# Performance work log

Hardware: AMD Instinct MI355X
Metric: run time of the kernel (lower is better)

The kernel has to match this reference:

```python
import jax, jax.numpy as jnp
import numpy as np

DIM = 1024
HID = 2048
E = 8
K = 2
INV_SQRT2 = 1.0 / 1.41421356237


def setup_inputs() -> dict:
    key = jax.random.key(0)
    ks = jax.random.split(key, 10)
    s = lambda fan_in: 1.0 / np.sqrt(fan_in)
    return {
        "x": jax.random.normal(ks[0], (4, 2048, DIM), dtype=jnp.float32),
        "gate_w": jax.random.uniform(ks[1], (DIM, E), jnp.float32, -s(DIM), s(DIM)),
        "gate_b": jnp.zeros((E,), jnp.float32),
        "w1": jax.random.uniform(ks[2], (E, DIM, HID), jnp.float32, -s(DIM), s(DIM)),
        "b1": jnp.zeros((E, HID), jnp.float32),
        "w2": jax.random.uniform(ks[3], (E, DIM, HID), jnp.float32, -s(DIM), s(DIM)),
        "b2": jnp.zeros((E, HID), jnp.float32),
        "w3": jax.random.uniform(ks[4], (E, HID, DIM), jnp.float32, -s(HID), s(HID)),
        "b3": jnp.zeros((E, DIM), jnp.float32),
    }


def reference(x, gate_w, gate_b, w1, b1, w2, b2, w3, b3):
    # Gating
    logits = jnp.einsum("bsd,de->bse", x, gate_w) + gate_b          # [b,s,E]
    scores = jax.nn.softmax(logits, axis=-1)
    topk_scores, topk_idx = jax.lax.top_k(scores, K)                  # [b,s,K]

    # Load-balance (entropy) loss over mean expert usage
    usage = scores.mean(axis=(0, 1))                                   # [E]
    lb_loss = -(usage * jnp.log(usage + 1e-9)).sum()

    # Per-token combine weight for each expert: score if expert in top-k else 0
    onehot = jax.nn.one_hot(topk_idx, E, dtype=x.dtype)               # [b,s,K,E]
    comb = (topk_scores[..., None] * onehot).sum(axis=2)              # [b,s,E]

    # SwiGLU experts (batched over E via einsum)
    h = jnp.einsum("bsd,edh->ebsh", x, w1) + b1[:, None, None, :]
    g = jax.nn.silu(jnp.einsum("bsd,edh->ebsh", x, w2) + b2[:, None, None, :])
    eo = jnp.einsum("ebsh,ehd->ebsd", h * g, w3) + b3[:, None, None, :]
    eo = eo * INV_SQRT2

    # Weighted combine (zero weight where expert not selected)
    out = jnp.einsum("ebsd,bse->bsd", eo, comb)
    return out, lb_loss
```

## Files before the change

kernel.cpp:

```cpp
#include <hip/hip_runtime.h>
#include <cstdio>

#define NTOK 8192
#define DIM 1024
#define HID 2048
#define NE 8
#define NPAIR (NTOK * 2)

typedef __attribute__((ext_vector_type(8))) short bf16x8;
typedef __attribute__((ext_vector_type(4))) float f32x4;

typedef const __attribute__((address_space(1))) void* gas_ptr;
typedef __attribute__((address_space(3))) void* las_ptr;

__device__ __forceinline__ void async16(const void* g, void* s) {
  __builtin_amdgcn_global_load_lds((gas_ptr)g, (las_ptr)s, 16, 0, 0);
}

__device__ __forceinline__ unsigned short f2bf(float f) {
  unsigned int u = __float_as_uint(f);
  u = (u + 0x7fff + ((u >> 16) & 1)) >> 16;
  return (unsigned short)u;
}

__device__ __forceinline__ float bf2f(unsigned short u) {
  return __uint_as_float((unsigned int)u << 16);
}


__global__ __launch_bounds__(256) void prep_kernel(
    const float* __restrict__ w1, const float* __restrict__ w2,
    const float* __restrict__ w3, unsigned short* __restrict__ w1bt,
    unsigned short* __restrict__ w2bt, unsigned short* __restrict__ w3bt) {
  const int z = blockIdx.y;
  const int m = z >> 3, e = z & 7;
  int R, C;
  const float* in;
  unsigned short* outp;
  if (m == 0)      { R = DIM; C = HID; in = w1; outp = w1bt; }
  else if (m == 1) { R = DIM; C = HID; in = w2; outp = w2bt; }
  else             { R = HID; C = DIM; in = w3; outp = w3bt; }
  in += (size_t)e * DIM * HID;
  outp += (size_t)e * DIM * HID;

  const int tilesx = C >> 5;
  const int c0 = (blockIdx.x % tilesx) * 32;
  const int r0 = (blockIdx.x / tilesx) * 32;

  __shared__ float tile[32][33];
  const int c = threadIdx.x & 31, rr = threadIdx.x >> 5;
#pragma unroll
  for (int i = 0; i < 4; i++) {
    const int r = rr + i * 8;
    tile[r][c] = in[(size_t)(r0 + r) * C + c0 + c];
  }
  __syncthreads();
#pragma unroll
  for (int i = 0; i < 4; i++) {
    const int cc2 = rr + i * 8;
    outp[(size_t)(c0 + cc2) * R + r0 + c] = f2bf(tile[c][cc2]);
  }
}

__global__ __launch_bounds__(256) void gate_kernel(
    const float* __restrict__ x, const float* __restrict__ gw,
    const float* __restrict__ gb, unsigned short* __restrict__ xb,
    float* __restrict__ scores, int* __restrict__ route_e,
    float* __restrict__ route_w) {
  __shared__ float sgwT[NE][DIM];
  const int tid = threadIdx.x;
#pragma unroll
  for (int i = 0; i < 8; i++) {
    const int j = i * 256 + tid;
    const float4 v = ((const float4*)gw)[j];
    const int d = j >> 1, e0 = (j & 1) * 4;
    sgwT[e0 + 0][d] = v.x; sgwT[e0 + 1][d] = v.y;
    sgwT[e0 + 2][d] = v.z; sgwT[e0 + 3][d] = v.w;
  }
  __syncthreads();

  const int wv = tid >> 6, lane = tid & 63;
  const int t = blockIdx.x * 4 + wv;
  float acc[NE] = {0.f, 0.f, 0.f, 0.f, 0.f, 0.f, 0.f, 0.f};
  const float4* x4 = (const float4*)(x + (size_t)t * DIM);
#pragma unroll
  for (int i = 0; i < 4; i++) {
    const float4 xv = x4[i * 64 + lane];
    const int d4 = i * 64 + lane;
    ushort4 xbv;
    xbv.x = f2bf(xv.x); xbv.y = f2bf(xv.y);
    xbv.z = f2bf(xv.z); xbv.w = f2bf(xv.w);
    *(ushort4*)(xb + (size_t)t * DIM + d4 * 4) = xbv;
#pragma unroll
    for (int e = 0; e < NE; e++) {
      const float4 wv4 = *(const float4*)&sgwT[e][d4 * 4];
      acc[e] += xv.x * wv4.x + xv.y * wv4.y + xv.z * wv4.z + xv.w * wv4.w;
    }
  }
#pragma unroll
  for (int e = 0; e < NE; e++)
#pragma unroll
    for (int s = 32; s; s >>= 1) acc[e] += __shfl_xor(acc[e], s, 64);

  if (lane == 0) {
    float l[NE], m = -1e30f;
#pragma unroll
    for (int e = 0; e < NE; e++) { l[e] = acc[e] + gb[e]; m = fmaxf(m, l[e]); }
    float p[NE], sum = 0.f;
#pragma unroll
    for (int e = 0; e < NE; e++) { p[e] = __expf(l[e] - m); sum += p[e]; }
    const float inv = 1.f / sum;
    float s[NE];
#pragma unroll
    for (int e = 0; e < NE; e++) { s[e] = p[e] * inv; scores[t * NE + e] = s[e]; }
    int i1 = 0;
    for (int e = 1; e < NE; e++) if (s[e] > s[i1]) i1 = e;
    int i2 = -1;
    for (int e = 0; e < NE; e++) {
      if (e == i1) continue;
      if (i2 < 0 || s[e] > s[i2]) i2 = e;
    }
    route_e[t * 2] = i1; route_e[t * 2 + 1] = i2;
    route_w[t * 2] = s[i1]; route_w[t * 2 + 1] = s[i2];
  }
}

__global__ void finalize_kernel(const float* __restrict__ scores,
                                const int* __restrict__ route_e,
                                int* __restrict__ ctrl,
                                float* __restrict__ out_lb) {
  __shared__ float red[1024];
  __shared__ int hist[NE];
  const int tid = threadIdx.x;
  if (tid < NE) hist[tid] = 0;
  const int e = tid & 7, row = tid >> 3;
  float s = 0.f;
  for (int i = 0; i < 64; i++) s += scores[(size_t)(row + i * 128) * NE + e];
  red[tid] = s;
  __syncthreads();
#pragma unroll
  for (int i = 0; i < 16; i++)
    atomicAdd(&hist[route_e[i * 1024 + tid]], 1);
  for (int st = 512; st >= 8; st >>= 1) {
    __syncthreads();
    if (tid < st) red[tid] += red[tid + st];
  }
  __syncthreads();
  if (tid == 0) {
    float lb = 0.f;
    for (int ee = 0; ee < NE; ee++) {
      const float u = red[ee] * (1.f / 8192.f);
      lb -= u * __logf(u + 1e-9f);
    }
    *out_lb = lb;
    int o = 0;
    for (int ee = 0; ee < NE; ee++) {
      ctrl[ee] = hist[ee];
      ctrl[8 + ee] = o;
      ctrl[17 + ee] = o;
      o += hist[ee];
    }
    ctrl[16] = o;
  }
}

__global__ void scatter_kernel(const int* __restrict__ route_e,
                               const float* __restrict__ route_w,
                               int* __restrict__ ctrl,
                               int* __restrict__ tok_list,
                               float* __restrict__ pair_w,
                               int* __restrict__ pair_pos) {
  const int t = blockIdx.x * 256 + threadIdx.x;
  if (t >= NTOK) return;
#pragma unroll
  for (int k = 0; k < 2; k++) {
    const int e = route_e[t * 2 + k];
    const int p = atomicAdd(&ctrl[17 + e], 1);
    tok_list[p] = t;
    pair_w[p] = route_w[t * 2 + k] * 0.70710678118654752f;
    pair_pos[t * 2 + k] = p;
  }
}

__global__ __launch_bounds__(512) void stage1_kernel(
    const unsigned short* __restrict__ xb, const unsigned short* __restrict__ w1bt,
    const unsigned short* __restrict__ w2bt, const float* __restrict__ b1,
    const float* __restrict__ b2, const int* __restrict__ tok_list,
    const int* __restrict__ ctrl, unsigned short* __restrict__ act) {
  const int e = blockIdx.z;
  const int cnt = ctrl[e];
  const int ytile = blockIdx.y;
  if (ytile * 256 >= cnt) return;
  const int off = ctrl[8 + e];
  const int rows = min(256, cnt - ytile * 256);
  const int h0 = blockIdx.x * 128;

  __shared__ unsigned short sX[2][256 * 64];
  __shared__ unsigned short sW1[2][128 * 64];
  __shared__ unsigned short sW2[2][128 * 64];

  const int tid = threadIdx.x;
  const int wv = tid >> 6, lane = tid & 63;
  const int rr = tid >> 3;
  const int c8 = ((tid & 7) ^ (rr & 7)) * 8;

  const unsigned short* w1p = w1bt + (size_t)e * HID * DIM + (size_t)h0 * DIM;
  const unsigned short* w2p = w2bt + (size_t)e * HID * DIM + (size_t)h0 * DIM;
  const unsigned short* gx[4];
  const unsigned short* gw1[2];
  const unsigned short* gw2[2];
#pragma unroll
  for (int r = 0; r < 4; r++)
    gx[r] = xb + (size_t)tok_list[off + ytile * 256 + min(rr + r * 64, rows - 1)] * DIM + c8;
#pragma unroll
  for (int r = 0; r < 2; r++) {
    gw1[r] = w1p + (size_t)(rr + r * 64) * DIM + c8;
    gw2[r] = w2p + (size_t)(rr + r * 64) * DIM + c8;
  }

  f32x4 ah[8][2], ag[8][2];
#pragma unroll
  for (int i = 0; i < 8; i++)
#pragma unroll
    for (int j = 0; j < 2; j++) {
      ah[i][j] = (f32x4){0.f, 0.f, 0.f, 0.f};
      ag[i][j] = (f32x4){0.f, 0.f, 0.f, 0.f};
    }

  const int wr = wv >> 2, wc = wv & 3;
  const int l15 = lane & 15, q = lane >> 4, r7 = lane & 7;

#pragma unroll
  for (int r = 0; r < 4; r++) {
    async16(gx[r], sX[0] + (r * 512 + wv * 64) * 8);
    gx[r] += 64;
  }
#pragma unroll
  for (int r = 0; r < 2; r++) {
    async16(gw1[r], sW1[0] + (r * 512 + wv * 64) * 8);
    async16(gw2[r], sW2[0] + (r * 512 + wv * 64) * 8);
    gw1[r] += 64; gw2[r] += 64;
  }
  __syncthreads();

  const int NT = DIM / 64;
  for (int t = 0; t < NT; t++) {
    const int cur = t & 1;
    if (t + 1 < NT) {
#pragma unroll
      for (int r = 0; r < 4; r++) {
        async16(gx[r], sX[cur ^ 1] + (r * 512 + wv * 64) * 8);
        gx[r] += 64;
      }
#pragma unroll
      for (int r = 0; r < 2; r++) {
        async16(gw1[r], sW1[cur ^ 1] + (r * 512 + wv * 64) * 8);
        async16(gw2[r], sW2[cur ^ 1] + (r * 512 + wv * 64) * 8);
        gw1[r] += 64; gw2[r] += 64;
      }
    }
#pragma unroll
    for (int kk = 0; kk < 2; kk++) {
      const int pch = ((kk * 4 + q) ^ r7) * 8;
      bf16x8 bx[8], a1[2], a2[2];
#pragma unroll
      for (int i = 0; i < 8; i++)
        bx[i] = *(const bf16x8*)(sX[cur] + (wr * 128 + i * 16 + l15) * 64 + pch);
#pragma unroll
      for (int j = 0; j < 2; j++) {
        a1[j] = *(const bf16x8*)(sW1[cur] + (wc * 32 + j * 16 + l15) * 64 + pch);
        a2[j] = *(const bf16x8*)(sW2[cur] + (wc * 32 + j * 16 + l15) * 64 + pch);
      }
#pragma unroll
      for (int i = 0; i < 8; i++)
#pragma unroll
        for (int j = 0; j < 2; j++) {
          ah[i][j] = __builtin_amdgcn_mfma_f32_16x16x32_bf16(a1[j], bx[i], ah[i][j], 0, 0, 0);
          ag[i][j] = __builtin_amdgcn_mfma_f32_16x16x32_bf16(a2[j], bx[i], ag[i][j], 0, 0, 0);
        }
    }
    __syncthreads();
  }

  f32x4 b1v[2], b2v[2];
#pragma unroll
  for (int j = 0; j < 2; j++) {
    const int hc = h0 + wc * 32 + j * 16 + q * 4;
    b1v[j] = *(const f32x4*)(b1 + e * HID + hc);
    b2v[j] = *(const f32x4*)(b2 + e * HID + hc);
  }
#pragma unroll
  for (int i = 0; i < 8; i++) {
    const int trow = wr * 128 + i * 16 + l15;
    if (trow < rows) {
      const size_t gp = (size_t)(off + ytile * 256 + trow) * HID;
#pragma unroll
      for (int j = 0; j < 2; j++) {
        const int hc = h0 + wc * 32 + j * 16 + q * 4;
        ushort4 o;
        {
          const float hh = ah[i][j][0] + b1v[j][0];
          const float gg = ag[i][j][0] + b2v[j][0];
          o.x = f2bf(hh * (gg / (1.f + __expf(-gg))));
        }
        {
          const float hh = ah[i][j][1] + b1v[j][1];
          const float gg = ag[i][j][1] + b2v[j][1];
          o.y = f2bf(hh * (gg / (1.f + __expf(-gg))));
        }
        {
          const float hh = ah[i][j][2] + b1v[j][2];
          const float gg = ag[i][j][2] + b2v[j][2];
          o.z = f2bf(hh * (gg / (1.f + __expf(-gg))));
        }
        {
          const float hh = ah[i][j][3] + b1v[j][3];
          const float gg = ag[i][j][3] + b2v[j][3];
          o.w = f2bf(hh * (gg / (1.f + __expf(-gg))));
        }
        *(ushort4*)(act + gp + hc) = o;
      }
    }
  }
}

__global__ __launch_bounds__(512) void stage2s_kernel(
    const unsigned short* __restrict__ act, const unsigned short* __restrict__ w3bt,
    const float* __restrict__ b3, const float* __restrict__ pair_w,
    const int* __restrict__ ctrl, unsigned short* __restrict__ pair_out) {
  const int e = blockIdx.z;
  const int cnt = ctrl[e];
  const int ytile = blockIdx.y;
  if (ytile * 256 >= cnt) return;
  const int off = ctrl[8 + e];
  const int rows = min(256, cnt - ytile * 256);
  const int d0 = blockIdx.x * 256;
  const int rbase = off + ytile * 256;

  __shared__ unsigned short sA[2][256 * 64];
  __shared__ unsigned short sW[2][256 * 64];

  const int tid = threadIdx.x;
  const int wv = tid >> 6, lane = tid & 63;
  const int rr = tid >> 3;
  const int c8 = ((tid & 7) ^ (rr & 7)) * 8;
  const unsigned short* w3p = w3bt + (size_t)e * DIM * HID + (size_t)d0 * HID;
  const unsigned short* ga[4];
  const unsigned short* gw[4];
#pragma unroll
  for (int r = 0; r < 4; r++) {
    const int row = rr + r * 64;
    ga[r] = act + (size_t)(rbase + min(row, rows - 1)) * HID + c8;
    gw[r] = w3p + (size_t)row * HID + c8;
  }

  f32x4 acc[8][4];
#pragma unroll
  for (int i = 0; i < 8; i++)
#pragma unroll
    for (int j = 0; j < 4; j++) acc[i][j] = (f32x4){0.f, 0.f, 0.f, 0.f};

  const int wr = wv >> 2, wc = wv & 3;
  const int l15 = lane & 15, q = lane >> 4, r7 = lane & 7;

#pragma unroll
  for (int r = 0; r < 4; r++) {
    async16(ga[r], sA[0] + (r * 512 + wv * 64) * 8);
    async16(gw[r], sW[0] + (r * 512 + wv * 64) * 8);
    ga[r] += 64; gw[r] += 64;
  }
  __syncthreads();

  const int NT = HID / 64;
  for (int t = 0; t < NT; t++) {
    const int cur = t & 1;
    if (t + 1 < NT) {
#pragma unroll
      for (int r = 0; r < 4; r++) {
        async16(ga[r], sA[cur ^ 1] + (r * 512 + wv * 64) * 8);
        async16(gw[r], sW[cur ^ 1] + (r * 512 + wv * 64) * 8);
        ga[r] += 64; gw[r] += 64;
      }
    }
#pragma unroll
    for (int kk = 0; kk < 2; kk++) {
      const int pch = ((kk * 4 + q) ^ r7) * 8;
      bf16x8 af[8], bf[4];
#pragma unroll
      for (int i = 0; i < 8; i++)
        af[i] = *(const bf16x8*)(sA[cur] + (wr * 128 + i * 16 + l15) * 64 + pch);
#pragma unroll
      for (int j = 0; j < 4; j++)
        bf[j] = *(const bf16x8*)(sW[cur] + (wc * 64 + j * 16 + l15) * 64 + pch);
#pragma unroll
      for (int i = 0; i < 8; i++)
#pragma unroll
        for (int j = 0; j < 4; j++)
          acc[i][j] =
              __builtin_amdgcn_mfma_f32_16x16x32_bf16(af[i], bf[j], acc[i][j], 0, 0, 0);
    }
    __syncthreads();
  }

#pragma unroll
  for (int i = 0; i < 8; i++)
#pragma unroll
    for (int rg = 0; rg < 4; rg++) {
      const int row = wr * 128 + i * 16 + q * 4 + rg;
      if (row < rows) {
        const int pr = rbase + row;
        const float wt = pair_w[pr];
#pragma unroll
        for (int j = 0; j < 4; j++) {
          const int dcol = d0 + wc * 64 + j * 16 + l15;
          pair_out[(size_t)pr * DIM + dcol] = f2bf((acc[i][j][rg] + b3[e * DIM + dcol]) * wt);
        }
      }
    }
}

__global__ __launch_bounds__(512) void stage2a_kernel(
    const unsigned short* __restrict__ act, const unsigned short* __restrict__ w3bt,
    const float* __restrict__ b3, const int* __restrict__ tok_list,
    const float* __restrict__ pair_w, const int* __restrict__ ctrl,
    float* __restrict__ out) {
  const int e = blockIdx.z;
  const int cnt = ctrl[e];
  const int ytile = blockIdx.y;
  if (ytile * 256 >= cnt) return;
  const int off = ctrl[8 + e];
  const int rows = min(256, cnt - ytile * 256);
  const int d0 = blockIdx.x * 256;
  const int rbase = off + ytile * 256;

  __shared__ unsigned short sA[2][256 * 64];
  __shared__ unsigned short sW[2][256 * 64];

  const int tid = threadIdx.x;
  const int wv = tid >> 6, lane = tid & 63;
  const int rr = tid >> 3;
  const int c8 = ((tid & 7) ^ (rr & 7)) * 8;
  const unsigned short* w3p = w3bt + (size_t)e * DIM * HID + (size_t)d0 * HID;
  const unsigned short* ga[4];
  const unsigned short* gw[4];
#pragma unroll
  for (int r = 0; r < 4; r++) {
    const int row = rr + r * 64;
    ga[r] = act + (size_t)(rbase + min(row, rows - 1)) * HID + c8;
    gw[r] = w3p + (size_t)row * HID + c8;
  }

  f32x4 acc[8][4];
#pragma unroll
  for (int i = 0; i < 8; i++)
#pragma unroll
    for (int j = 0; j < 4; j++) acc[i][j] = (f32x4){0.f, 0.f, 0.f, 0.f};

  const int wr = wv >> 2, wc = wv & 3;
  const int l15 = lane & 15, q = lane >> 4, r7 = lane & 7;

#pragma unroll
  for (int r = 0; r < 4; r++) {
    async16(ga[r], sA[0] + (r * 512 + wv * 64) * 8);
    async16(gw[r], sW[0] + (r * 512 + wv * 64) * 8);
    ga[r] += 64; gw[r] += 64;
  }
  __syncthreads();

  const int NT = HID / 64;
  for (int t = 0; t < NT; t++) {
    const int cur = t & 1;
    if (t + 1 < NT) {
#pragma unroll
      for (int r = 0; r < 4; r++) {
        async16(ga[r], sA[cur ^ 1] + (r * 512 + wv * 64) * 8);
        async16(gw[r], sW[cur ^ 1] + (r * 512 + wv * 64) * 8);
        ga[r] += 64; gw[r] += 64;
      }
    }
#pragma unroll
    for (int kk = 0; kk < 2; kk++) {
      const int pch = ((kk * 4 + q) ^ r7) * 8;
      bf16x8 af[8], bf[4];
#pragma unroll
      for (int i = 0; i < 8; i++)
        af[i] = *(const bf16x8*)(sA[cur] + (wr * 128 + i * 16 + l15) * 64 + pch);
#pragma unroll
      for (int j = 0; j < 4; j++)
        bf[j] = *(const bf16x8*)(sW[cur] + (wc * 64 + j * 16 + l15) * 64 + pch);
#pragma unroll
      for (int i = 0; i < 8; i++)
#pragma unroll
        for (int j = 0; j < 4; j++)
          acc[i][j] =
              __builtin_amdgcn_mfma_f32_16x16x32_bf16(af[i], bf[j], acc[i][j], 0, 0, 0);
    }
    __syncthreads();
  }

#pragma unroll
  for (int i = 0; i < 8; i++)
#pragma unroll
    for (int rg = 0; rg < 4; rg++) {
      const int row = wr * 128 + i * 16 + q * 4 + rg;
      if (row < rows) {
        const int pr = rbase + row;
        const int tok = tok_list[pr];
        const float wt = pair_w[pr];
#pragma unroll
        for (int j = 0; j < 4; j++) {
          const int dcol = d0 + wc * 64 + j * 16 + l15;
          atomicAdd(out + (size_t)tok * DIM + dcol, (acc[i][j][rg] + b3[e * DIM + dcol]) * wt);
        }
      }
    }
}

__global__ __launch_bounds__(256) void combine_kernel(
    const unsigned short* __restrict__ pair_out, const int* __restrict__ pair_pos,
    float* __restrict__ out) {
  const int t = blockIdx.x;
  const int d = threadIdx.x * 4;
  const int p0 = pair_pos[t * 2], p1 = pair_pos[t * 2 + 1];
  const ushort4 a = *(const ushort4*)(pair_out + (size_t)p0 * DIM + d);
  const ushort4 b = *(const ushort4*)(pair_out + (size_t)p1 * DIM + d);
  float4 r;
  r.x = bf2f(a.x) + bf2f(b.x);
  r.y = bf2f(a.y) + bf2f(b.y);
  r.z = bf2f(a.z) + bf2f(b.z);
  r.w = bf2f(a.w) + bf2f(b.w);
  *(float4*)(out + (size_t)t * DIM + d) = r;
}

static const size_t SZ_XB  = (size_t)NTOK * DIM * 2;
static const size_t SZ_W   = (size_t)NE * DIM * HID * 2;
static const size_t SZ_ACT = (size_t)NPAIR * HID * 2;
static const size_t OFF_XB  = 0;
static const size_t OFF_W1  = OFF_XB + SZ_XB;
static const size_t OFF_W2  = OFF_W1 + SZ_W;
static const size_t OFF_W3  = OFF_W2 + SZ_W;
static const size_t OFF_ACT = OFF_W3 + SZ_W;
static const size_t OFF_SC  = OFF_ACT + SZ_ACT;
static const size_t OFF_RE  = OFF_SC + (size_t)NTOK * NE * 4;
static const size_t OFF_RW  = OFF_RE + (size_t)NPAIR * 4;
static const size_t OFF_TL  = OFF_RW + (size_t)NPAIR * 4;
static const size_t OFF_PW  = OFF_TL + (size_t)NPAIR * 4;
static const size_t OFF_PP  = OFF_PW + (size_t)NPAIR * 4;
static const size_t OFF_CT  = OFF_PP + (size_t)NPAIR * 4;
static const size_t WS_BASE = OFF_CT + 128;
static const size_t OFF_PO  = WS_BASE;
static const size_t WS_FULL = OFF_PO + (size_t)NPAIR * DIM * 2;

extern "C" void kernel_launch(void* const* d_in, const int* in_sizes, int n_in,
                              void* d_out, int out_size, void* d_ws, size_t ws_size,
                              hipStream_t stream) {
  const float* x      = (const float*)d_in[0];
  const float* gate_w = (const float*)d_in[1];
  const float* gate_b = (const float*)d_in[2];
  const float* w1     = (const float*)d_in[3];
  const float* b1     = (const float*)d_in[4];
  const float* w2     = (const float*)d_in[5];
  const float* b2     = (const float*)d_in[6];
  const float* w3     = (const float*)d_in[7];
  const float* b3     = (const float*)d_in[8];
  float* out = (float*)d_out;

  if (ws_size < WS_BASE) {
    fprintf(stderr, "kernel_launch: ws_size %zu < needed %zu\n", ws_size, WS_BASE);
    return;
  }
  const bool store_path = (ws_size >= WS_FULL);

  char* ws = (char*)d_ws;
  unsigned short* xb   = (unsigned short*)(ws + OFF_XB);
  unsigned short* w1bt = (unsigned short*)(ws + OFF_W1);
  unsigned short* w2bt = (unsigned short*)(ws + OFF_W2);
  unsigned short* w3bt = (unsigned short*)(ws + OFF_W3);
  unsigned short* act  = (unsigned short*)(ws + OFF_ACT);
  float* scores        = (float*)(ws + OFF_SC);
  int* route_e         = (int*)(ws + OFF_RE);
  float* route_w       = (float*)(ws + OFF_RW);
  int* tok_list        = (int*)(ws + OFF_TL);
  float* pair_w        = (float*)(ws + OFF_PW);
  int* pair_pos        = (int*)(ws + OFF_PP);
  int* ctrl            = (int*)(ws + OFF_CT);
  unsigned short* pout = (unsigned short*)(ws + OFF_PO);

  if (!store_path)
    hipMemsetAsync(d_out, 0, (size_t)out_size * sizeof(float), stream);

  prep_kernel<<<dim3(2048, 24), 256, 0, stream>>>(w1, w2, w3, w1bt, w2bt, w3bt);
  gate_kernel<<<2048, 256, 0, stream>>>(x, gate_w, gate_b, xb, scores, route_e,
                                        route_w);
  finalize_kernel<<<1, 1024, 0, stream>>>(scores, route_e, ctrl, out + (out_size - 1));
  scatter_kernel<<<32, 256, 0, stream>>>(route_e, route_w, ctrl, tok_list, pair_w,
                                         pair_pos);
  stage1_kernel<<<dim3(16, 32, 8), 512, 0, stream>>>(xb, w1bt, w2bt, b1, b2,
                                                     tok_list, ctrl, act);
  if (store_path) {
    stage2s_kernel<<<dim3(4, 32, 8), 512, 0, stream>>>(act, w3bt, b3, pair_w, ctrl, pout);
    combine_kernel<<<NTOK, 256, 0, stream>>>(pout, pair_pos, out);
  } else {
    stage2a_kernel<<<dim3(4, 32, 8), 512, 0, stream>>>(act, w3bt, b3, tok_list,
                                                       pair_w, ctrl, out);
  }
}
```

Measured before the change: 659.8 us.

## Deepen GEMM pipelines to four-stage K=32 async loads with explicit waitcnt barriers

Rewrites the main loops of the stage1 and stage2 expert GEMMs. The old loop used two-stage double buffering over K=64 with __syncthreads. The new loop uses a four-buffer ring of K=32 slices prefetched three steps ahead, with a matching 32-column XOR swizzle. Synchronisation now uses raw s_barrier plus explicit vmcnt/lgkmcnt waits, and s_setprio raises priority around the MFMA block, so global loads overlap compute more deeply and block-wide stalls are reduced. The risks are more barriers per unit of work and fragile hand-counted waitcnt values that could race if miscounted.

```diff
diff --git a/kernel.cpp b/kernel.cpp
--- a/kernel.cpp
+++ b/kernel.cpp
@@ -27,6 +27,11 @@
   return __uint_as_float((unsigned int)u << 16);
 }
 
+
+#define S_BARRIER __builtin_amdgcn_s_barrier()
+#define VM_WAIT(N) asm volatile("s_waitcnt vmcnt(" #N ")" ::: "memory")
+#define LGKM0 asm volatile("s_waitcnt lgkmcnt(0)" ::: "memory")
+#define CFENCE asm volatile("" ::: "memory")
 
 __global__ __launch_bounds__(256) void prep_kernel(
     const float* __restrict__ w1, const float* __restrict__ w2,
@@ -195,28 +200,23 @@
   const int rows = min(256, cnt - ytile * 256);
   const int h0 = blockIdx.x * 128;
 
-  __shared__ unsigned short sX[2][256 * 64];
-  __shared__ unsigned short sW1[2][128 * 64];
-  __shared__ unsigned short sW2[2][128 * 64];
+  __shared__ unsigned short sX[4][256 * 32];
+  __shared__ unsigned short sW1[4][128 * 32];
+  __shared__ unsigned short sW2[4][128 * 32];
 
   const int tid = threadIdx.x;
   const int wv = tid >> 6, lane = tid & 63;
-  const int rr = tid >> 3;
-  const int c8 = ((tid & 7) ^ (rr & 7)) * 8;
+
+  const int cl = ((tid & 3) ^ ((tid >> 3) & 3)) * 8;
 
   const unsigned short* w1p = w1bt + (size_t)e * HID * DIM + (size_t)h0 * DIM;
   const unsigned short* w2p = w2bt + (size_t)e * HID * DIM + (size_t)h0 * DIM;
-  const unsigned short* gx[4];
-  const unsigned short* gw1[2];
-  const unsigned short* gw2[2];
-#pragma unroll
-  for (int r = 0; r < 4; r++)
-    gx[r] = xb + (size_t)tok_list[off + ytile * 256 + min(rr + r * 64, rows - 1)] * DIM + c8;
-#pragma unroll
-  for (int r = 0; r < 2; r++) {
-    gw1[r] = w1p + (size_t)(rr + r * 64) * DIM + c8;
-    gw2[r] = w2p + (size_t)(rr + r * 64) * DIM + c8;
-  }
+  const unsigned short* gx0 =
+      xb + (size_t)tok_list[off + ytile * 256 + min(tid >> 2, rows - 1)] * DIM + cl;
+  const unsigned short* gx1 =
+      xb + (size_t)tok_list[off + ytile * 256 + min(128 + (tid >> 2), rows - 1)] * DIM + cl;
+  const unsigned short* gw1 = w1p + (size_t)(tid >> 2) * DIM + cl;
+  const unsigned short* gw2 = w2p + (size_t)(tid >> 2) * DIM + cl;
 
   f32x4 ah[8][2], ag[8][2];
 #pragma unroll
@@ -228,59 +228,63 @@
     }
 
   const int wr = wv >> 2, wc = wv & 3;
-  const int l15 = lane & 15, q = lane >> 4, r7 = lane & 7;
-
-#pragma unroll
-  for (int r = 0; r < 4; r++) {
-    async16(gx[r], sX[0] + (r * 512 + wv * 64) * 8);
-    gx[r] += 64;
-  }
-#pragma unroll
-  for (int r = 0; r < 2; r++) {
-    async16(gw1[r], sW1[0] + (r * 512 + wv * 64) * 8);
-    async16(gw2[r], sW2[0] + (r * 512 + wv * 64) * 8);
-    gw1[r] += 64; gw2[r] += 64;
-  }
-  __syncthreads();
-
-  const int NT = DIM / 64;
+  const int l15 = lane & 15, q = lane >> 4;
+  const int pch = (q ^ ((l15 >> 1) & 3)) * 8;
+
+#define S1_STAGE(B)                                   \
+  do {                                                \
+    async16(gx0, sX[B] + (wv * 64) * 8);              \
+    async16(gx1, sX[B] + (512 + wv * 64) * 8);        \
+    async16(gw1, sW1[B] + (wv * 64) * 8);             \
+    async16(gw2, sW2[B] + (wv * 64) * 8);             \
+    gx0 += 32; gx1 += 32; gw1 += 32; gw2 += 32;       \
+  } while (0)
+
+  S1_STAGE(0); S1_STAGE(1); S1_STAGE(2);
+  VM_WAIT(8);
+  S_BARRIER;
+  CFENCE;
+
+  const int NT = DIM / 32;
   for (int t = 0; t < NT; t++) {
-    const int cur = t & 1;
-    if (t + 1 < NT) {
-#pragma unroll
-      for (int r = 0; r < 4; r++) {
-        async16(gx[r], sX[cur ^ 1] + (r * 512 + wv * 64) * 8);
-        gx[r] += 64;
+    const int cur = t & 3;
+    bf16x8 bx[8], a1[2], a2[2];
+    {
+      const unsigned short* xs = sX[cur];
+      const unsigned short* w1s = sW1[cur];
+      const unsigned short* w2s = sW2[cur];
+#pragma unroll
+      for (int i = 0; i < 8; i++)
+        bx[i] = *(const bf16x8*)(xs + (wr * 128 + i * 16 + l15) * 32 + pch);
+#pragma unroll
+      for (int j = 0; j < 2; j++) {
+        a1[j] = *(const bf16x8*)(w1s + (wc * 32 + j * 16 + l15) * 32 + pch);
+        a2[j] = *(const bf16x8*)(w2s + (wc * 32 + j * 16 + l15) * 32 + pch);
       }
-#pragma unroll
-      for (int r = 0; r < 2; r++) {
-        async16(gw1[r], sW1[cur ^ 1] + (r * 512 + wv * 64) * 8);
-        async16(gw2[r], sW2[cur ^ 1] + (r * 512 + wv * 64) * 8);
-        gw1[r] += 64; gw2[r] += 64;
-      }
-    }
-#pragma unroll
-    for (int kk = 0; kk < 2; kk++) {
-      const int pch = ((kk * 4 + q) ^ r7) * 8;
-      bf16x8 bx[8], a1[2], a2[2];
-#pragma unroll
-      for (int i = 0; i < 8; i++)
-        bx[i] = *(const bf16x8*)(sX[cur] + (wr * 128 + i * 16 + l15) * 64 + pch);
-#pragma unroll
-      for (int j = 0; j < 2; j++) {
-        a1[j] = *(const bf16x8*)(sW1[cur] + (wc * 32 + j * 16 + l15) * 64 + pch);
-        a2[j] = *(const bf16x8*)(sW2[cur] + (wc * 32 + j * 16 + l15) * 64 + pch);
-      }
-#pragma unroll
-      for (int i = 0; i < 8; i++)
-#pragma unroll
-        for (int j = 0; j < 2; j++) {
-          ah[i][j] = __builtin_amdgcn_mfma_f32_16x16x32_bf16(a1[j], bx[i], ah[i][j], 0, 0, 0);
-          ag[i][j] = __builtin_amdgcn_mfma_f32_16x16x32_bf16(a2[j], bx[i], ag[i][j], 0, 0, 0);
-        }
-    }
-    __syncthreads();
-  }
+    }
+    if (t < NT - 3) {
+      const int nb = (t + 3) & 3;
+      S1_STAGE(nb);
+    }
+    S_BARRIER;
+    LGKM0;
+    __builtin_amdgcn_sched_barrier(0);
+    __builtin_amdgcn_s_setprio(1);
+#pragma unroll
+    for (int i = 0; i < 8; i++) {
+      ah[i][0] = __builtin_amdgcn_mfma_f32_16x16x32_bf16(a1[0], bx[i], ah[i][0], 0, 0, 0);
+      ag[i][0] = __builtin_amdgcn_mfma_f32_16x16x32_bf16(a2[0], bx[i], ag[i][0], 0, 0, 0);
+      ah[i][1] = __builtin_amdgcn_mfma_f32_16x16x32_bf16(a1[1], bx[i], ah[i][1], 0, 0, 0);
+      ag[i][1] = __builtin_amdgcn_mfma_f32_16x16x32_bf16(a2[1], bx[i], ag[i][1], 0, 0, 0);
+    }
+    __builtin_amdgcn_s_setprio(0);
+    if (t < NT - 3) VM_WAIT(8);
+    else if (t == NT - 3) VM_WAIT(4);
+    else if (t == NT - 2) VM_WAIT(0);
+    CFENCE;
+    S_BARRIER;
+  }
+#undef S1_STAGE
 
   f32x4 b1v[2], b2v[2];
 #pragma unroll
@@ -337,22 +341,20 @@
   const int d0 = blockIdx.x * 256;
   const int rbase = off + ytile * 256;
 
-  __shared__ unsigned short sA[2][256 * 64];
-  __shared__ unsigned short sW[2][256 * 64];
+  __shared__ unsigned short sA[4][256 * 32];
+  __shared__ unsigned short sW[4][256 * 32];
 
   const int tid = threadIdx.x;
   const int wv = tid >> 6, lane = tid & 63;
-  const int rr = tid >> 3;
-  const int c8 = ((tid & 7) ^ (rr & 7)) * 8;
+  const int cl = ((tid & 3) ^ ((tid >> 3) & 3)) * 8;
+
   const unsigned short* w3p = w3bt + (size_t)e * DIM * HID + (size_t)d0 * HID;
-  const unsigned short* ga[4];
-  const unsigned short* gw[4];
-#pragma unroll
-  for (int r = 0; r < 4; r++) {
-    const int row = rr + r * 64;
-    ga[r] = act + (size_t)(rbase + min(row, rows - 1)) * HID + c8;
-    gw[r] = w3p + (size_t)row * HID + c8;
-  }
+  const unsigned short* ga0 =
+      act + (size_t)(rbase + min(tid >> 2, rows - 1)) * HID + cl;
+  const unsigned short* ga1 =
+      act + (size_t)(rbase + min(128 + (tid >> 2), rows - 1)) * HID + cl;
+  const unsigned short* gw0 = w3p + (size_t)(tid >> 2) * HID + cl;
+  const unsigned short* gw1 = w3p + (size_t)(128 + (tid >> 2)) * HID + cl;
 
   f32x4 acc[8][4];
 #pragma unroll
@@ -361,46 +363,59 @@
     for (int j = 0; j < 4; j++) acc[i][j] = (f32x4){0.f, 0.f, 0.f, 0.f};
 
   const int wr = wv >> 2, wc = wv & 3;
-  const int l15 = lane & 15, q = lane >> 4, r7 = lane & 7;
-
-#pragma unroll
-  for (int r = 0; r < 4; r++) {
-    async16(ga[r], sA[0] + (r * 512 + wv * 64) * 8);
-    async16(gw[r], sW[0] + (r * 512 + wv * 64) * 8);
-    ga[r] += 64; gw[r] += 64;
-  }
-  __syncthreads();
-
-  const int NT = HID / 64;
+  const int l15 = lane & 15, q = lane >> 4;
+  const int pch = (q ^ ((l15 >> 1) & 3)) * 8;
+
+#define S2_STAGE(B)                                   \
+  do {                                                \
+    async16(ga0, sA[B] + (wv * 64) * 8);              \
+    async16(ga1, sA[B] + (512 + wv * 64) * 8);        \
+    async16(gw0, sW[B] + (wv * 64) * 8);              \
+    async16(gw1, sW[B] + (512 + wv * 64) * 8);        \
+    ga0 += 32; ga1 += 32; gw0 += 32; gw1 += 32;       \
+  } while (0)
+
+  S2_STAGE(0); S2_STAGE(1); S2_STAGE(2);
+  VM_WAIT(8);
+  S_BARRIER;
+  CFENCE;
+
+  const int NT = HID / 32;
   for (int t = 0; t < NT; t++) {
-    const int cur = t & 1;
-    if (t + 1 < NT) {
-#pragma unroll
-      for (int r = 0; r < 4; r++) {
-        async16(ga[r], sA[cur ^ 1] + (r * 512 + wv * 64) * 8);
-        async16(gw[r], sW[cur ^ 1] + (r * 512 + wv * 64) * 8);
-        ga[r] += 64; gw[r] += 64;
-      }
-    }
-#pragma unroll
-    for (int kk = 0; kk < 2; kk++) {
-      const int pch = ((kk * 4 + q) ^ r7) * 8;
-      bf16x8 af[8], bf[4];
+    const int cur = t & 3;
+    bf16x8 af[8], bf[4];
+    {
+      const unsigned short* as = sA[cur];
+      const unsigned short* ws = sW[cur];
 #pragma unroll
       for (int i = 0; i < 8; i++)
-        af[i] = *(const bf16x8*)(sA[cur] + (wr * 128 + i * 16 + l15) * 64 + pch);
+        af[i] = *(const bf16x8*)(as + (wr * 128 + i * 16 + l15) * 32 + pch);
 #pragma unroll
       for (int j = 0; j < 4; j++)
-        bf[j] = *(const bf16x8*)(sW[cur] + (wc * 64 + j * 16 + l15) * 64 + pch);
-#pragma unroll
-      for (int i = 0; i < 8; i++)
-#pragma unroll
-        for (int j = 0; j < 4; j++)
-          acc[i][j] =
-              __builtin_amdgcn_mfma_f32_16x16x32_bf16(af[i], bf[j], acc[i][j], 0, 0, 0);
-    }
-    __syncthreads();
-  }
+        bf[j] = *(const bf16x8*)(ws + (wc * 64 + j * 16 + l15) * 32 + pch);
+    }
+    if (t < NT - 3) {
+      const int nb = (t + 3) & 3;
+      S2_STAGE(nb);
+    }
+    S_BARRIER;
+    LGKM0;
+    __builtin_amdgcn_sched_barrier(0);
+    __builtin_amdgcn_s_setprio(1);
+#pragma unroll
+    for (int i = 0; i < 8; i++)
+#pragma unroll
+      for (int j = 0; j < 4; j++)
+        acc[i][j] =
+            __builtin_amdgcn_mfma_f32_16x16x32_bf16(af[i], bf[j], acc[i][j], 0, 0, 0);
+    __builtin_amdgcn_s_setprio(0);
+    if (t < NT - 3) VM_WAIT(8);
+    else if (t == NT - 3) VM_WAIT(4);
+    else if (t == NT - 2) VM_WAIT(0);
+    CFENCE;
+    S_BARRIER;
+  }
+#undef S2_STAGE
 
 #pragma unroll
   for (int i = 0; i < 8; i++)
@@ -433,22 +448,20 @@
   const int d0 = blockIdx.x * 256;
   const int rbase = off + ytile * 256;
 
-  __shared__ unsigned short sA[2][256 * 64];
-  __shared__ unsigned short sW[2][256 * 64];
+  __shared__ unsigned short sA[4][256 * 32];
+  __shared__ unsigned short sW[4][256 * 32];
 
   const int tid = threadIdx.x;
   const int wv = tid >> 6, lane = tid & 63;
-  const int rr = tid >> 3;
-  const int c8 = ((tid & 7) ^ (rr & 7)) * 8;
+  const int cl = ((tid & 3) ^ ((tid >> 3) & 3)) * 8;
+
   const unsigned short* w3p = w3bt + (size_t)e * DIM * HID + (size_t)d0 * HID;
-  const unsigned short* ga[4];
-  const unsigned short* gw[4];
-#pragma unroll
-  for (int r = 0; r < 4; r++) {
-    const int row = rr + r * 64;
-    ga[r] = act + (size_t)(rbase + min(row, rows - 1)) * HID + c8;
-    gw[r] = w3p + (size_t)row * HID + c8;
-  }
+  const unsigned short* ga0 =
+      act + (size_t)(rbase + min(tid >> 2, rows - 1)) * HID + cl;
+  const unsigned short* ga1 =
+      act + (size_t)(rbase + min(128 + (tid >> 2), rows - 1)) * HID + cl;
+  const unsigned short* gw0 = w3p + (size_t)(tid >> 2) * HID + cl;
+  const unsigned short* gw1 = w3p + (size_t)(128 + (tid >> 2)) * HID + cl;
 
   f32x4 acc[8][4];
 #pragma unroll
@@ -457,46 +470,59 @@
     for (int j = 0; j < 4; j++) acc[i][j] = (f32x4){0.f, 0.f, 0.f, 0.f};
 
   const int wr = wv >> 2, wc = wv & 3;
-  const int l15 = lane & 15, q = lane >> 4, r7 = lane & 7;
-
-#pragma unroll
-  for (int r = 0; r < 4; r++) {
-    async16(ga[r], sA[0] + (r * 512 + wv * 64) * 8);
-    async16(gw[r], sW[0] + (r * 512 + wv * 64) * 8);
-    ga[r] += 64; gw[r] += 64;
-  }
-  __syncthreads();
-
-  const int NT = HID / 64;
+  const int l15 = lane & 15, q = lane >> 4;
+  const int pch = (q ^ ((l15 >> 1) & 3)) * 8;
+
+#define S2A_STAGE(B)                                  \
+  do {                                                \
+    async16(ga0, sA[B] + (wv * 64) * 8);              \
+    async16(ga1, sA[B] + (512 + wv * 64) * 8);        \
+    async16(gw0, sW[B] + (wv * 64) * 8);              \
+    async16(gw1, sW[B] + (512 + wv * 64) * 8);        \
+    ga0 += 32; ga1 += 32; gw0 += 32; gw1 += 32;       \
+  } while (0)
+
+  S2A_STAGE(0); S2A_STAGE(1); S2A_STAGE(2);
+  VM_WAIT(8);
+  S_BARRIER;
+  CFENCE;
+
+  const int NT = HID / 32;
   for (int t = 0; t < NT; t++) {
-    const int cur = t & 1;
-    if (t + 1 < NT) {
-#pragma unroll
-      for (int r = 0; r < 4; r++) {
-        async16(ga[r], sA[cur ^ 1] + (r * 512 + wv * 64) * 8);
-        async16(gw[r], sW[cur ^ 1] + (r * 512 + wv * 64) * 8);
-        ga[r] += 64; gw[r] += 64;
-      }
-    }
-#pragma unroll
-    for (int kk = 0; kk < 2; kk++) {
-      const int pch = ((kk * 4 + q) ^ r7) * 8;
-      bf16x8 af[8], bf[4];
+    const int cur = t & 3;
+    bf16x8 af[8], bf[4];
+    {
+      const unsigned short* as = sA[cur];
+      const unsigned short* ws = sW[cur];
 #pragma unroll
       for (int i = 0; i < 8; i++)
-        af[i] = *(const bf16x8*)(sA[cur] + (wr * 128 + i * 16 + l15) * 64 + pch);
+        af[i] = *(const bf16x8*)(as + (wr * 128 + i * 16 + l15) * 32 + pch);
 #pragma unroll
       for (int j = 0; j < 4; j++)
-        bf[j] = *(const bf16x8*)(sW[cur] + (wc * 64 + j * 16 + l15) * 64 + pch);
-#pragma unroll
-      for (int i = 0; i < 8; i++)
-#pragma unroll
-        for (int j = 0; j < 4; j++)
-          acc[i][j] =
-              __builtin_amdgcn_mfma_f32_16x16x32_bf16(af[i], bf[j], acc[i][j], 0, 0, 0);
-    }
-    __syncthreads();
-  }
+        bf[j] = *(const bf16x8*)(ws + (wc * 64 + j * 16 + l15) * 32 + pch);
+    }
+    if (t < NT - 3) {
+      const int nb = (t + 3) & 3;
+      S2A_STAGE(nb);
+    }
+    S_BARRIER;
+    LGKM0;
+    __builtin_amdgcn_sched_barrier(0);
+    __builtin_amdgcn_s_setprio(1);
+#pragma unroll
+    for (int i = 0; i < 8; i++)
+#pragma unroll
+      for (int j = 0; j < 4; j++)
+        acc[i][j] =
+            __builtin_amdgcn_mfma_f32_16x16x32_bf16(af[i], bf[j], acc[i][j], 0, 0, 0);
+    __builtin_amdgcn_s_setprio(0);
+    if (t < NT - 3) VM_WAIT(8);
+    else if (t == NT - 3) VM_WAIT(4);
+    else if (t == NT - 2) VM_WAIT(0);
+    CFENCE;
+    S_BARRIER;
+  }
+#undef S2A_STAGE
 
 #pragma unroll
   for (int i = 0; i < 8; i++)
```

Measured after the change: 640.9 us. 2.9% less time.
